# Kernel optimization log

Hardware: AMD Instinct MI355X
Metric: run time of the kernel (lower is better)

The kernel has to match this reference:

```python
import jax, jax.numpy as jnp
import numpy as np
from jax import lax

B, N, C = 4, 16384, 128
HEADS = 2
SR = 4
EPS = 1e-6


def setup_inputs() -> dict:
    key = jax.random.key(0)
    ks = jax.random.split(key, 6)
    s = 0.02
    return {
        "x": jax.random.normal(ks[0], (B, N, C), jnp.float32),
        "Wq": jax.random.normal(ks[1], (C, C), jnp.float32) * s,
        "Wk": jax.random.normal(ks[2], (C, C), jnp.float32) * s,
        "Wv": jax.random.normal(ks[3], (C, C), jnp.float32) * s,
        "Wproj": jax.random.normal(ks[4], (C, C), jnp.float32) * s,
        "sr_kernel": jax.random.normal(ks[5], (SR, SR, C, C), jnp.float32) * s,
        "sr_bias": jnp.zeros((C,), jnp.float32),
        "gamma": jnp.ones((C,), jnp.float32),
        "beta": jnp.zeros((C,), jnp.float32),
    }


def reference(x, Wq, Wk, Wv, Wproj, sr_kernel, sr_bias, gamma, beta):
    b, n, c = x.shape
    h = w = int(np.sqrt(n))          # H = W = sqrt(N), static
    dh = c // HEADS                  # head dim
    scale = dh ** -0.5

    # Q projection -> (B, heads, N, dh)
    q = (x @ Wq).reshape(b, n, HEADS, dh).transpose(0, 2, 1, 3)

    # Spatial reduction of K/V: conv stride=SR, 'same' padding, then LayerNorm
    x_img = x.reshape(b, h, w, c)
    x_ = lax.conv_general_dilated(
        x_img, sr_kernel, window_strides=(SR, SR), padding="SAME",
        dimension_numbers=("NHWC", "HWIO", "NHWC"))
    x_ = x_ + sr_bias
    x_ = x_.reshape(b, -1, c)        # (B, N', C), N' = (H/SR)*(W/SR)
    mu = jnp.mean(x_, axis=-1, keepdims=True)
    var = jnp.mean(jnp.square(x_ - mu), axis=-1, keepdims=True)
    x_ = (x_ - mu) * lax.rsqrt(var + EPS) * gamma + beta

    k = (x_ @ Wk).reshape(b, -1, HEADS, dh).transpose(0, 2, 1, 3)  # (B,h,N',dh)
    v = (x_ @ Wv).reshape(b, -1, HEADS, dh).transpose(0, 2, 1, 3)

    attn = jnp.einsum("bhqd,bhkd->bhqk", q, k) * scale
    attn = jax.nn.softmax(attn, axis=-1)
    out = jnp.einsum("bhqk,bhkd->bhqd", attn, v)
    out = out.transpose(0, 2, 1, 3).reshape(b, n, c)
    return out @ Wproj
```

## Files before the change

kernel.cpp:

```cpp
#include <hip/hip_runtime.h>
#include <hip/hip_bf16.h>

typedef unsigned short u16;
typedef __attribute__((ext_vector_type(8))) short short8;
typedef __attribute__((ext_vector_type(4))) float f32x4;
typedef __attribute__((ext_vector_type(2))) float f32x2;

#define MFMA16(a, b, c) __builtin_amdgcn_mfma_f32_16x16x32_bf16((a), (b), (c), 0, 0, 0)

__device__ __forceinline__ u16 f2bf(float f) {
  __hip_bfloat16 h = __float2bfloat16(f);
  u16 r;
  __builtin_memcpy(&r, &h, 2);
  return r;
}
__device__ __forceinline__ float bf2f(u16 h) {
  unsigned u = ((unsigned)h) << 16;
  float f;
  __builtin_memcpy(&f, &u, 4);
  return f;
}
__device__ __forceinline__ unsigned pk2(float a, float b) {
  return (unsigned)f2bf(a) | ((unsigned)f2bf(b) << 16);
}
__device__ __forceinline__ short8 ld8(const void* src, int idx, int isf32) {
  short8 v;
  if (isf32) {
    const float4* s = (const float4*)((const float*)src + idx);
    float4 p0 = s[0], p1 = s[1];
    v[0] = (short)f2bf(p0.x); v[1] = (short)f2bf(p0.y);
    v[2] = (short)f2bf(p0.z); v[3] = (short)f2bf(p0.w);
    v[4] = (short)f2bf(p1.x); v[5] = (short)f2bf(p1.y);
    v[6] = (short)f2bf(p1.z); v[7] = (short)f2bf(p1.w);
  } else {
    v = *(const short8*)((const u16*)src + idx);
  }
  return v;
}
__device__ __forceinline__ float ld1(const void* src, int idx, int isf32) {
  return isf32 ? ((const float*)src)[idx] : bf2f(((const u16*)src)[idx]);
}
__device__ __forceinline__ int detect_isf32(const u16* xw) {
  int lane = threadIdx.x & 63;
  int cnt = 0;
#pragma unroll
  for (int i = 0; i < 16; ++i) {
    u16 w = xw[lane * 16 + i];
    cnt += (((w >> 7) & 0xFF) >= 0xC0) ? 1 : 0;
  }
#pragma unroll
  for (int off = 1; off < 64; off <<= 1) cnt += __shfl_xor(cnt, off, 64);
  return cnt >= 32;
}

__global__ void prep_kernel(const void* __restrict__ srk, const void* __restrict__ Wq,
                            const void* __restrict__ Wk, const void* __restrict__ Wv,
                            const void* __restrict__ Wp, const void* __restrict__ x,
                            u16* __restrict__ WcT) {
  const int isf32 = detect_isf32((const u16*)x);
  int gid = blockIdx.x * 256 + threadIdx.x;
  if (gid >= 327680) return;
  int cout = (gid >> 7) & 127, cin = gid & 127;
  float v;
  if (gid < 262144) {
    int mat = gid >> 14;
    v = ld1(srk, mat * 16384 + cin * 128 + cout, isf32);
  } else {
    int mat = (gid - 262144) >> 14;
    const void* src = (mat == 0) ? Wq : (mat == 1) ? Wk : (mat == 2) ? Wv : Wp;
    v = ld1(src, cin * 128 + cout, isf32);
  }
  WcT[gid] = f2bf(v);
}

__launch_bounds__(1024, 4)
__global__ void conv_ln_kv_kernel(const void* __restrict__ x, const u16* __restrict__ wcT,
                                  const void* __restrict__ sr_bias,
                                  const void* __restrict__ gamma,
                                  const void* __restrict__ beta,
                                  const u16* __restrict__ WkT, const u16* __restrict__ WvT,
                                  u16* __restrict__ Kb, u16* __restrict__ Vt) {
  extern __shared__ char cws[];
  float* Racc = (float*)cws;
  u16* Xs = (u16*)(cws + 16 * 16 * 128 * 4);
  const int isf32 = detect_isf32((const u16*)x);
  const int tid = threadIdx.x;
  const int wave = tid >> 6, lane = tid & 63;
  const int quad = lane >> 4, l16 = lane & 15;
  const int g = blockIdx.x;

  const int row = g * 16 + l16;
  const int pb = row >> 10, rem = row & 1023, oh = rem >> 5, ow = rem & 31;
  const int xbase = ((pb * 128 + oh * 4) * 128 + ow * 4) * 128;

  f32x4 acc[8];
#pragma unroll
  for (int i = 0; i < 8; ++i) acc[i] = (f32x4){0.f, 0.f, 0.f, 0.f};

  {
    const int r = wave >> 2, sc = wave & 3;
    short8 a[4];
#pragma unroll
    for (int kc = 0; kc < 4; ++kc)
      a[kc] = ld8(x, xbase + r * 16384 + sc * 128 + kc * 32 + quad * 8, isf32);
#pragma unroll
    for (int nt = 0; nt < 8; ++nt)
#pragma unroll
      for (int kc = 0; kc < 4; ++kc) {
        short8 bw = *(const short8*)(wcT + wave * 16384 + (nt * 16 + l16) * 128 +
                                     kc * 32 + quad * 8);
        acc[nt] = MFMA16(a[kc], bw, acc[nt]);
      }
  }
#pragma unroll
  for (int nt = 0; nt < 8; ++nt)
#pragma unroll
    for (int rr = 0; rr < 4; ++rr)
      Racc[(wave * 16 + quad * 4 + rr) * 128 + nt * 16 + l16] = acc[nt][rr];
  __syncthreads();

  {
    const int lrow = wave, c0 = lane * 2;
    f32x2 rsum = (f32x2){0.f, 0.f};
#pragma unroll
    for (int w = 0; w < 16; ++w) {
      f32x2 t = *(const f32x2*)&Racc[(w * 16 + lrow) * 128 + c0];
      rsum[0] += t[0];
      rsum[1] += t[1];
    }
    float v0 = rsum[0] + ld1(sr_bias, c0, isf32);
    float v1 = rsum[1] + ld1(sr_bias, c0 + 1, isf32);
    float sum = v0 + v1, sum2 = v0 * v0 + v1 * v1;
#pragma unroll
    for (int off = 1; off < 64; off <<= 1) {
      sum += __shfl_xor(sum, off, 64);
      sum2 += __shfl_xor(sum2, off, 64);
    }
    const float mu = sum * (1.f / 128.f);
    const float var = sum2 * (1.f / 128.f) - mu * mu;
    const float rinv = rsqrtf(fmaxf(var, 0.f) + 1e-6f);
    float y0 = (v0 - mu) * rinv * ld1(gamma, c0, isf32) + ld1(beta, c0, isf32);
    float y1 = (v1 - mu) * rinv * ld1(gamma, c0 + 1, isf32) + ld1(beta, c0 + 1, isf32);
    *(unsigned*)&Xs[lrow * 136 + c0] = pk2(y0, y1);
  }
  __syncthreads();

  short8 a2[4];
#pragma unroll
  for (int kc = 0; kc < 4; ++kc)
    a2[kc] = *(const short8*)&Xs[l16 * 136 + kc * 32 + quad * 8];
  const u16* Wm = (wave & 1) ? WvT : WkT;
  const int nt = wave >> 1;
  f32x4 a3 = (f32x4){0.f, 0.f, 0.f, 0.f};
#pragma unroll
  for (int kc = 0; kc < 4; ++kc) {
    short8 bm = *(const short8*)(Wm + (nt * 16 + l16) * 128 + kc * 32 + quad * 8);
    a3 = MFMA16(a2[kc], bm, a3);
  }
#pragma unroll
  for (int rr = 0; rr < 4; ++rr) {
    const int rowg = g * 16 + quad * 4 + rr;
    const int b = rowg >> 10, key = rowg & 1023;
    const int c = nt * 16 + l16;
    if (wave & 1)
      Vt[(b * 128 + c) * 1024 + key] = f2bf(a3[rr]);
    else
      Kb[rowg * 128 + c] = f2bf(a3[rr]);
  }
}

__launch_bounds__(512, 4)
__global__ void attn_kernel(const void* __restrict__ x, const u16* __restrict__ WqT,
                            const u16* __restrict__ WpT, const u16* __restrict__ Kb,
                            const u16* __restrict__ Vt, float* __restrict__ out) {
  extern __shared__ u16 lds[];
  u16* Ks = lds;
  u16* Vs = Ks + 64 * 136;
  u16* Pa = Vs + 128 * 72;
  const int isf32 = detect_isf32((const u16*)x);
  const int tid = threadIdx.x;
  const int wave = tid >> 6, lane = tid & 63;
  const int quad = lane >> 4, l16 = lane & 15;
  const int b = blockIdx.x >> 7;
  const int row0 = (blockIdx.x & 127) * 128;
  const int wrow = wave * 16;
  u16* Pw = Pa + wave * 2176;

  const float qscale = 0.125f * 1.4426950408889634f;

  short8 qf[2][2];
  {
    short8 xb[4];
#pragma unroll
    for (int kc = 0; kc < 4; ++kc)
      xb[kc] = ld8(x, (b * 16384 + row0 + wrow + l16) * 128 + kc * 32 + quad * 8, isf32);
#pragma unroll
    for (int nt = 0; nt < 8; ++nt) {
      f32x4 qa = (f32x4){0.f, 0.f, 0.f, 0.f};
#pragma unroll
      for (int kc = 0; kc < 4; ++kc) {
        short8 w = *(const short8*)(WqT + (nt * 16 + l16) * 128 + kc * 32 + quad * 8);
        qa = MFMA16(w, xb[kc], qa);
      }
      uint2 pk = {pk2(qa[0] * qscale, qa[1] * qscale), pk2(qa[2] * qscale, qa[3] * qscale)};
      *(uint2*)&Pw[l16 * 136 + nt * 16 + quad * 4] = pk;
    }
#pragma unroll
    for (int h = 0; h < 2; ++h)
#pragma unroll
      for (int k0 = 0; k0 < 2; ++k0)
        qf[h][k0] = *(const short8*)&Pw[l16 * 136 + h * 64 + k0 * 32 + quad * 8];
  }

  f32x4 o[2][4];
#pragma unroll
  for (int h = 0; h < 2; ++h)
#pragma unroll
    for (int nt = 0; nt < 4; ++nt) o[h][nt] = (f32x4){0.f, 0.f, 0.f, 0.f};
  float l[2] = {0.f, 0.f};

  const int kkey = tid >> 3, kseg = tid & 7;
  const int vc = tid >> 2, vseg = tid & 3;

  for (int ch = 0; ch < 16; ++ch) {
    __syncthreads();
    {
      const uint4* src = (const uint4*)(Kb + (b * 1024 + ch * 64 + kkey) * 128 + kseg * 16);
      uint4* dst = (uint4*)&Ks[kkey * 136 + kseg * 16];
      dst[0] = src[0];
      dst[1] = src[1];
    }
    {
      const uint4* src = (const uint4*)(Vt + (b * 128 + vc) * 1024 + ch * 64 + vseg * 16);
      uint4* dst = (uint4*)&Vs[vc * 72 + vseg * 16];
      dst[0] = src[0];
      dst[1] = src[1];
    }
    __syncthreads();
#pragma unroll
    for (int h = 0; h < 2; ++h) {
#pragma unroll
      for (int ct = 0; ct < 4; ++ct) {
        short8 kf0 = *(const short8*)&Ks[(ct * 16 + l16) * 136 + h * 64 + quad * 8];
        short8 kf1 = *(const short8*)&Ks[(ct * 16 + l16) * 136 + h * 64 + 32 + quad * 8];
        f32x4 s0 = (f32x4){0.f, 0.f, 0.f, 0.f};
        s0 = MFMA16(kf0, qf[h][0], s0);
        s0 = MFMA16(kf1, qf[h][1], s0);
        float p0 = exp2f(s0[0]), p1 = exp2f(s0[1]), p2 = exp2f(s0[2]), p3 = exp2f(s0[3]);
        l[h] += (p0 + p1) + (p2 + p3);
        uint2 pka = {pk2(p0, p1), pk2(p2, p3)};
        *(uint2*)&Pw[l16 * 72 + ct * 16 + quad * 4] = pka;
      }
#pragma unroll
      for (int kc = 0; kc < 2; ++kc) {
        short8 pf0 = *(const short8*)&Pw[l16 * 72 + kc * 32 + quad * 8];
#pragma unroll
        for (int nt = 0; nt < 4; ++nt) {
          short8 vf = *(const short8*)&Vs[(h * 64 + nt * 16 + l16) * 72 + kc * 32 + quad * 8];
          o[h][nt] = MFMA16(vf, pf0, o[h][nt]);
        }
      }
    }
  }

#pragma unroll
  for (int h = 0; h < 2; ++h) {
    float t = l[h];
    t += __shfl_xor(t, 16, 64);
    t += __shfl_xor(t, 32, 64);
    const float inv = 1.0f / t;
#pragma unroll
    for (int nt = 0; nt < 4; ++nt)
#pragma unroll
      for (int rr = 0; rr < 4; ++rr) o[h][nt][rr] *= inv;
  }

  {
#pragma unroll
    for (int h = 0; h < 2; ++h)
#pragma unroll
      for (int nt = 0; nt < 4; ++nt) {
        uint2 pk = {pk2(o[h][nt][0], o[h][nt][1]), pk2(o[h][nt][2], o[h][nt][3])};
        *(uint2*)&Pw[l16 * 136 + h * 64 + nt * 16 + quad * 4] = pk;
      }
    short8 of[4];
#pragma unroll
    for (int kc = 0; kc < 4; ++kc)
      of[kc] = *(const short8*)&Pw[l16 * 136 + kc * 32 + quad * 8];
#pragma unroll
    for (int nt = 0; nt < 8; ++nt) {
      f32x4 pa = (f32x4){0.f, 0.f, 0.f, 0.f};
#pragma unroll
      for (int kc = 0; kc < 4; ++kc) {
        short8 w = *(const short8*)(WpT + (nt * 16 + l16) * 128 + kc * 32 + quad * 8);
        pa = MFMA16(of[kc], w, pa);
      }
#pragma unroll
      for (int rr = 0; rr < 4; ++rr)
        out[(b * 16384 + row0 + wrow + quad * 4 + rr) * 128 + nt * 16 + l16] = pa[rr];
    }
  }
}

extern "C" void kernel_launch(void* const* d_in, const int* in_sizes, int n_in,
                              void* d_out, int out_size, void* d_ws, size_t ws_size,
                              hipStream_t stream) {
  (void)in_sizes; (void)n_in; (void)out_size; (void)ws_size;
  const void* x = d_in[0];
  const void* Wq = d_in[1];
  const void* Wk = d_in[2];
  const void* Wv = d_in[3];
  const void* Wp = d_in[4];
  const void* srk = d_in[5];
  const void* sbias = d_in[6];
  const void* gamma = d_in[7];
  const void* beta = d_in[8];
  float* out = (float*)d_out;
  u16* ws = (u16*)d_ws;

  u16* WcT = ws;
  u16* WqT = ws + 262144;
  u16* WkT = ws + 278528;
  u16* WvT = ws + 294912;
  u16* WpT = ws + 311296;
  u16* Kb = ws + 327680;
  u16* Vt = ws + 851968;

  prep_kernel<<<dim3(1280), dim3(256), 0, stream>>>(srk, Wq, Wk, Wv, Wp, x, WcT);
  conv_ln_kv_kernel<<<dim3(256), dim3(1024), 16 * 16 * 128 * 4 + 16 * 136 * 2, stream>>>(
      x, WcT, sbias, gamma, beta, WkT, WvT, Kb, Vt);
  attn_kernel<<<dim3(512), dim3(512), (64 * 136 + 128 * 72 + 8 * 2176) * 2, stream>>>(
      x, WqT, WpT, Kb, Vt, out);
}
```

Baseline: 214.7 us.

## Prefetch K/V chunks into registers, shrink LDS footprint, swizzle blocks, set MFMA priority

New measurement: 215.3 us. No clear change (+0.3%).

```diff
diff --git a/kernel.cpp b/kernel.cpp
--- a/kernel.cpp
+++ b/kernel.cpp
@@ -176,17 +176,28 @@
   extern __shared__ u16 lds[];
   u16* Ks = lds;
   u16* Vs = Ks + 64 * 136;
-  u16* Pa = Vs + 128 * 72;
+  u16* Pp = Vs + 128 * 72;
   const int isf32 = detect_isf32((const u16*)x);
   const int tid = threadIdx.x;
   const int wave = tid >> 6, lane = tid & 63;
   const int quad = lane >> 4, l16 = lane & 15;
-  const int b = blockIdx.x >> 7;
-  const int row0 = (blockIdx.x & 127) * 128;
+  const int swz = (blockIdx.x & 7) * 64 + (blockIdx.x >> 3);
+  const int b = swz >> 7;
+  const int row0 = (swz & 127) * 128;
   const int wrow = wave * 16;
-  u16* Pw = Pa + wave * 2176;
+  u16* Pw = Pp + wave * 1152;
+  u16* Fw = lds + wave * 2176;
 
   const float qscale = 0.125f * 1.4426950408889634f;
+
+  const int kkey = tid >> 3, kseg = tid & 7;
+  const int vc = tid >> 2, vseg = tid & 3;
+  const u16* ksrc = Kb + (b * 1024 + kkey) * 128 + kseg * 16;
+  const u16* vsrc = Vt + (b * 128 + vc) * 1024 + vseg * 16;
+  uint4 krg0 = *(const uint4*)ksrc;
+  uint4 krg1 = *(const uint4*)(ksrc + 8);
+  uint4 vrg0 = *(const uint4*)vsrc;
+  uint4 vrg1 = *(const uint4*)(vsrc + 8);
 
   short8 qf[2][2];
   {
@@ -203,14 +214,15 @@
         qa = MFMA16(w, xb[kc], qa);
       }
       uint2 pk = {pk2(qa[0] * qscale, qa[1] * qscale), pk2(qa[2] * qscale, qa[3] * qscale)};
-      *(uint2*)&Pw[l16 * 136 + nt * 16 + quad * 4] = pk;
+      *(uint2*)&Fw[l16 * 136 + nt * 16 + quad * 4] = pk;
     }
 #pragma unroll
     for (int h = 0; h < 2; ++h)
 #pragma unroll
       for (int k0 = 0; k0 < 2; ++k0)
-        qf[h][k0] = *(const short8*)&Pw[l16 * 136 + h * 64 + k0 * 32 + quad * 8];
-  }
+        qf[h][k0] = *(const short8*)&Fw[l16 * 136 + h * 64 + k0 * 32 + quad * 8];
+  }
+  __syncthreads();
 
   f32x4 o[2][4];
 #pragma unroll
@@ -219,24 +231,22 @@
     for (int nt = 0; nt < 4; ++nt) o[h][nt] = (f32x4){0.f, 0.f, 0.f, 0.f};
   float l[2] = {0.f, 0.f};
 
-  const int kkey = tid >> 3, kseg = tid & 7;
-  const int vc = tid >> 2, vseg = tid & 3;
-
   for (int ch = 0; ch < 16; ++ch) {
+    {
+      uint4* kd = (uint4*)&Ks[kkey * 136 + kseg * 16];
+      kd[0] = krg0;
+      kd[1] = krg1;
+      uint4* vd = (uint4*)&Vs[vc * 72 + vseg * 16];
+      vd[0] = vrg0;
+      vd[1] = vrg1;
+    }
     __syncthreads();
-    {
-      const uint4* src = (const uint4*)(Kb + (b * 1024 + ch * 64 + kkey) * 128 + kseg * 16);
-      uint4* dst = (uint4*)&Ks[kkey * 136 + kseg * 16];
-      dst[0] = src[0];
-      dst[1] = src[1];
-    }
-    {
-      const uint4* src = (const uint4*)(Vt + (b * 128 + vc) * 1024 + ch * 64 + vseg * 16);
-      uint4* dst = (uint4*)&Vs[vc * 72 + vseg * 16];
-      dst[0] = src[0];
-      dst[1] = src[1];
-    }
-    __syncthreads();
+    if (ch < 15) {
+      krg0 = *(const uint4*)(ksrc + (ch + 1) * 8192);
+      krg1 = *(const uint4*)(ksrc + (ch + 1) * 8192 + 8);
+      vrg0 = *(const uint4*)(vsrc + (ch + 1) * 64);
+      vrg1 = *(const uint4*)(vsrc + (ch + 1) * 64 + 8);
+    }
 #pragma unroll
     for (int h = 0; h < 2; ++h) {
 #pragma unroll
@@ -251,6 +261,7 @@
         uint2 pka = {pk2(p0, p1), pk2(p2, p3)};
         *(uint2*)&Pw[l16 * 72 + ct * 16 + quad * 4] = pka;
       }
+      __builtin_amdgcn_s_setprio(1);
 #pragma unroll
       for (int kc = 0; kc < 2; ++kc) {
         short8 pf0 = *(const short8*)&Pw[l16 * 72 + kc * 32 + quad * 8];
@@ -260,7 +271,9 @@
           o[h][nt] = MFMA16(vf, pf0, o[h][nt]);
         }
       }
-    }
+      __builtin_amdgcn_s_setprio(0);
+    }
+    __syncthreads();
   }
 
 #pragma unroll
@@ -281,12 +294,12 @@
 #pragma unroll
       for (int nt = 0; nt < 4; ++nt) {
         uint2 pk = {pk2(o[h][nt][0], o[h][nt][1]), pk2(o[h][nt][2], o[h][nt][3])};
-        *(uint2*)&Pw[l16 * 136 + h * 64 + nt * 16 + quad * 4] = pk;
+        *(uint2*)&Fw[l16 * 136 + h * 64 + nt * 16 + quad * 4] = pk;
       }
     short8 of[4];
 #pragma unroll
     for (int kc = 0; kc < 4; ++kc)
-      of[kc] = *(const short8*)&Pw[l16 * 136 + kc * 32 + quad * 8];
+      of[kc] = *(const short8*)&Fw[l16 * 136 + kc * 32 + quad * 8];
 #pragma unroll
     for (int nt = 0; nt < 8; ++nt) {
       f32x4 pa = (f32x4){0.f, 0.f, 0.f, 0.f};
@@ -329,6 +342,6 @@
   prep_kernel<<<dim3(1280), dim3(256), 0, stream>>>(srk, Wq, Wk, Wv, Wp, x, WcT);
   conv_ln_kv_kernel<<<dim3(256), dim3(1024), 16 * 16 * 128 * 4 + 16 * 136 * 2, stream>>>(
       x, WcT, sbias, gamma, beta, WkT, WvT, Kb, Vt);
-  attn_kernel<<<dim3(512), dim3(512), (64 * 136 + 128 * 72 + 8 * 2176) * 2, stream>>>(
+  attn_kernel<<<dim3(512), dim3(512), (64 * 136 + 128 * 72 + 8 * 1152) * 2, stream>>>(
       x, WqT, WpT, Kb, Vt, out);
 }
```
